# Kernel optimization log

Hardware: AMD Instinct MI355X
Metric: run time of the kernel (lower is better)

Reference implementation:

```python
import jax, jax.numpy as jnp
import numpy as np

EMBED_DIM = 256
NUM_HEADS = 8
NUM_LEVELS = 4
NUM_POINTS = 4
HEAD_DIM = EMBED_DIM // NUM_HEADS


def _bilinear_sample(img, x, y):
    """img: [N,C,H,W]; x,y: [N,P] absolute pixel coords (align_corners=False mapping
    already applied by caller). Zero padding outside, matching F.grid_sample."""
    N, C, H, W = img.shape
    x0 = jnp.floor(x)
    y0 = jnp.floor(y)
    wx1 = x - x0
    wy1 = y - y0
    img_flat = img.reshape(N, C, H * W)

    def gather(ix, iy):
        valid = ((ix >= 0) & (ix <= W - 1) & (iy >= 0) & (iy <= H - 1)).astype(img.dtype)
        idx = (jnp.clip(iy, 0, H - 1) * W + jnp.clip(ix, 0, W - 1)).astype(jnp.int32)
        v = jnp.take_along_axis(img_flat, idx[:, None, :], axis=2)  # [N,C,P]
        return v * valid[:, None, :]

    return (gather(x0, y0) * ((1.0 - wx1) * (1.0 - wy1))[:, None, :]
            + gather(x0 + 1.0, y0) * (wx1 * (1.0 - wy1))[:, None, :]
            + gather(x0, y0 + 1.0) * ((1.0 - wx1) * wy1)[:, None, :]
            + gather(x0 + 1.0, y0 + 1.0) * (wx1 * wy1)[:, None, :])


def _reference_points(H, W):
    yy, xx = jnp.meshgrid(jnp.arange(H, dtype=jnp.float32), jnp.arange(W, dtype=jnp.float32), indexing='ij')
    # stack order is (x, y), matching grid_sample's (x=width, y=height) convention
    return jnp.stack([(xx + 0.5) / W, (yy + 0.5) / H], axis=-1).reshape(H * W, 2)


def _frame_attention(q_feat, values, level_shapes, Wq, bq, Woff, boff, Wattn, battn, Wout, bout):
    Bt, C, H, W = q_feat.shape
    N = H * W
    q = q_feat.reshape(Bt, C, N).transpose(0, 2, 1) @ Wq + bq  # [Bt,N,C]
    off = (q @ Woff + boff).reshape(Bt, N, NUM_HEADS, NUM_LEVELS, NUM_POINTS, 2)
    aw = jax.nn.softmax((q @ Wattn + battn).reshape(Bt, N, NUM_HEADS, NUM_LEVELS * NUM_POINTS), axis=-1)
    aw = aw.reshape(Bt, N, NUM_HEADS, NUM_LEVELS, NUM_POINTS)
    ref = _reference_points(H, W)  # [N,2]
    sampled = []
    for l, (val, (Hl, Wl)) in enumerate(zip(values, level_shapes)):
        loc = ref[None, :, None, None, :] + off[:, :, :, l] / jnp.array([Wl, Hl], dtype=q.dtype)
        grid = jnp.clip(loc, 0.0, 1.0) * 2.0 - 1.0  # [Bt,N,M,K,2]
        grid = grid.transpose(0, 2, 1, 3, 4).reshape(Bt * NUM_HEADS, N * NUM_POINTS, 2)
        # align_corners=False: pixel = ((g+1)*size - 1)/2
        x = ((grid[..., 0] + 1.0) * Wl - 1.0) * 0.5
        y = ((grid[..., 1] + 1.0) * Hl - 1.0) * 0.5
        s = _bilinear_sample(val, x, y)  # [Bt*M, hd, N*K]
        s = s.reshape(Bt, NUM_HEADS, HEAD_DIM, N, NUM_POINTS).transpose(0, 3, 1, 4, 2)  # [Bt,N,M,K,hd]
        sampled.append(s)
    samp = jnp.stack(sampled, axis=3)  # [Bt,N,M,L,K,hd]
    out = (samp * aw[..., None]).sum(axis=(3, 4)).reshape(Bt, N, C)
    out = out @ Wout + bout
    return out.transpose(0, 2, 1).reshape(Bt, C, H, W)


def _forward(feats, Wq, bq, Wv, bv, Woff, boff, Wattn, battn, Wout, bout):
    B, C, H0, W0, T = feats[0].shape
    # original loops over frames t; frames are independent, so fold T into batch
    feats_bt = [jnp.moveaxis(f, -1, 1).reshape(f.shape[0] * T, C, f.shape[2], f.shape[3]) for f in feats]
    level_shapes = [(f.shape[2], f.shape[3]) for f in feats_bt]
    Bt = B * T
    # value projection per level (identical across query scales; compute once)
    values = []
    for f, (Hl, Wl) in zip(feats_bt, level_shapes):
        v = f.reshape(Bt, C, Hl * Wl).transpose(0, 2, 1) @ Wv + bv  # [Bt,HW,C]
        v = v.reshape(Bt, Hl * Wl, NUM_HEADS, HEAD_DIM).transpose(0, 2, 3, 1).reshape(Bt * NUM_HEADS, HEAD_DIM, Hl, Wl)
        values.append(v)
    outs = []
    for f, (Hl, Wl) in zip(feats_bt, level_shapes):
        o = _frame_attention(f, values, level_shapes, Wq, bq, Woff, boff, Wattn, battn, Wout, bout)
        outs.append(o.reshape(B, T, C, Hl, Wl).transpose(0, 2, 3, 4, 1))  # back to [B,C,H,W,T]
    return tuple(outs)


def setup_inputs() -> dict:
    key = jax.random.key(0)
    ks = jax.random.split(key, 10)
    B, T, C = 2, 2, EMBED_DIM
    shapes = [(64, 64), (32, 32), (16, 16), (8, 8)]
    inp = {}
    for i, (H, W) in enumerate(shapes):
        inp[f"feats{i}"] = jax.random.normal(ks[i], (B, C, H, W, T), dtype=jnp.float32)
    s = float(1.0 / np.sqrt(C))
    noff = NUM_HEADS * NUM_LEVELS * NUM_POINTS
    inp["Wq"] = jax.random.normal(ks[4], (C, C), jnp.float32) * s
    inp["bq"] = jnp.zeros((C,), jnp.float32)
    inp["Wv"] = jax.random.normal(ks[5], (C, C), jnp.float32) * s
    inp["bv"] = jnp.zeros((C,), jnp.float32)
    inp["Woff"] = jax.random.normal(ks[6], (C, noff * 2), jnp.float32) * 0.01
    inp["boff"] = jax.random.normal(ks[7], (noff * 2,), jnp.float32) * 2.0
    inp["Wattn"] = jax.random.normal(ks[8], (C, noff), jnp.float32) * 0.01
    inp["battn"] = jnp.zeros((noff,), jnp.float32)
    inp["Wout"] = jax.random.normal(ks[9], (C, C), jnp.float32) * s
    inp["bout"] = jnp.zeros((C,), jnp.float32)
    return inp


def reference(feats0, feats1, feats2, feats3, Wq, bq, Wv, bv, Woff, boff, Wattn, battn, Wout, bout):
    return _forward([feats0, feats1, feats2, feats3], Wq, bq, Wv, bv, Woff, boff, Wattn, battn, Wout, bout)
```

## Files before the change

kernel.cpp:

```cpp
#include <hip/hip_runtime.h>
#include <hip/hip_bf16.h>

#define NR 21760

typedef short short8 __attribute__((ext_vector_type(8)));
typedef float f32x4 __attribute__((ext_vector_type(4)));

__device__ __forceinline__ int level_of_row(int R) {
    if (R < 16384) return 0;
    if (R < 20480) return 1;
    if (R < 21504) return 2;
    return 3;
}

__global__ __launch_bounds__(256) void pack_all_kernel(const float* __restrict__ f0,
                                                       const float* __restrict__ f1,
                                                       const float* __restrict__ f2,
                                                       const float* __restrict__ f3,
                                                       __hip_bfloat16* __restrict__ XP) {
    int bx = blockIdx.x;
    const float* f; int nj, Wl, rowbase, rel;
    if (bx < 1024)      { f = f0; nj = 128; Wl = 64; rowbase = 0;     rel = bx; }
    else if (bx < 1280) { f = f1; nj = 32;  Wl = 32; rowbase = 16384; rel = bx - 1024; }
    else if (bx < 1344) { f = f2; nj = 8;   Wl = 16; rowbase = 20480; rel = bx - 1280; }
    else                { f = f3; nj = 2;   Wl = 8;  rowbase = 21504; rel = bx - 1344; }
    const int HW = Wl * Wl;
    const int HWT = HW * 2;
    const int j0 = (rel % nj) * 64;
    const int c0 = ((rel / nj) & 3) * 64;
    const int b  = rel / (nj * 4);
    __shared__ float tile[64][65];
    {
        const int tj = threadIdx.x & 63;
        const int tcb = threadIdx.x >> 6;
        const float* fb = f + (size_t)(b * 256 + c0) * HWT + j0;
#pragma unroll
        for (int i = 0; i < 16; ++i) {
            int cl = tcb + i * 4;
            tile[cl][tj] = fb[(size_t)cl * HWT + tj];
        }
    }
    __syncthreads();
    {
        const int tc = threadIdx.x & 63;
        const int tjb = threadIdx.x >> 6;
#pragma unroll
        for (int i = 0; i < 16; ++i) {
            int jl = tjb + i * 4;
            int j = j0 + jl;
            int p = j >> 1, t = j & 1;
            int row = rowbase + (b * 2 + t) * HW + p;
            XP[(size_t)row * 256 + c0 + tc] = __float2bfloat16(tile[tc][jl]);
        }
    }
}

__global__ __launch_bounds__(256) void wtrans_all_kernel(const float* __restrict__ Wq,
                                                         const float* __restrict__ Wv,
                                                         const float* __restrict__ Woff,
                                                         const float* __restrict__ Wattn,
                                                         const float* __restrict__ Wout,
                                                         const float* __restrict__ boff,
                                                         const float* __restrict__ battn,
                                                         __hip_bfloat16* __restrict__ WTvq,
                                                         __hip_bfloat16* __restrict__ WToa,
                                                         __hip_bfloat16* __restrict__ WTout,
                                                         float* __restrict__ bias_oa) {
    __shared__ float t[32][33];
    const int bx = blockIdx.x;
    const int tid = threadIdx.x;
    if (bx == 288) {
        bias_oa[tid] = boff[tid];
        if (tid < 128) bias_oa[256 + tid] = battn[tid];
        return;
    }
    const float* W; __hip_bfloat16* WT; int N; int rel;
    if (bx < 64)       { W = Wv;    WT = WTvq;             N = 256; rel = bx; }
    else if (bx < 128) { W = Wq;    WT = WTvq + 256 * 256; N = 256; rel = bx - 64; }
    else if (bx < 192) { W = Woff;  WT = WToa;             N = 256; rel = bx - 128; }
    else if (bx < 224) { W = Wattn; WT = WToa + 256 * 256; N = 128; rel = bx - 192; }
    else               { W = Wout;  WT = WTout;            N = 256; rel = bx - 224; }
    const int K = 256;
    const int ntiles = N >> 5;
    const int n0 = (rel % ntiles) * 32, k0 = (rel / ntiles) * 32;
    const int c = tid & 31, r = tid >> 5;
#pragma unroll
    for (int i = 0; i < 4; ++i)
        t[r + 8 * i][c] = W[(size_t)(k0 + r + 8 * i) * N + n0 + c];
    __syncthreads();
#pragma unroll
    for (int i = 0; i < 4; ++i)
        WT[(size_t)(n0 + r + 8 * i) * K + k0 + c] = __float2bfloat16(t[c][r + 8 * i]);
}

template <int OUTMODE>
__global__ __launch_bounds__(256) void gemm_mfma(const __hip_bfloat16* __restrict__ A,
                                                 const __hip_bfloat16* __restrict__ BT,
                                                 const float* __restrict__ bias,
                                                 const float* __restrict__ bias2,
                                                 void* __restrict__ Cout,
                                                 void* __restrict__ Cout2,
                                                 int M, int N, int K) {
    __shared__ __align__(16) __hip_bfloat16 As[64][72];
    __shared__ __align__(16) __hip_bfloat16 Bs[64][72];
    const int m0 = blockIdx.x * 64;
    const int n0 = blockIdx.y * 64;
    const int w = threadIdx.x >> 6;
    const int lane = threadIdx.x & 63;
    const int wm = (w >> 1) * 32;
    const int wn = (w & 1) * 32;
    const int fr = lane & 15;
    const int fq = lane >> 4;
    const int srow = threadIdx.x >> 3;
    const int schunk = threadIdx.x & 7;
    f32x4 acc[2][2] = {};

    for (int kt = 0; kt < K; kt += 64) {
        __syncthreads();
#pragma unroll
        for (int i = 0; i < 2; ++i) {
            int r = srow + 32 * i;
            float4 va = *(const float4*)(&A[(size_t)(m0 + r) * K + kt + schunk * 8]);
            *(float4*)(&As[r][schunk * 8]) = va;
            float4 vb = *(const float4*)(&BT[(size_t)(n0 + r) * K + kt + schunk * 8]);
            *(float4*)(&Bs[r][schunk * 8]) = vb;
        }
        __syncthreads();
#pragma unroll
        for (int ks = 0; ks < 2; ++ks) {
            short8 a[2], b[2];
#pragma unroll
            for (int fi = 0; fi < 2; ++fi)
                a[fi] = *(const short8*)(&As[wm + fi * 16 + fr][ks * 32 + fq * 8]);
#pragma unroll
            for (int fj = 0; fj < 2; ++fj)
                b[fj] = *(const short8*)(&Bs[wn + fj * 16 + fr][ks * 32 + fq * 8]);
#pragma unroll
            for (int fi = 0; fi < 2; ++fi)
#pragma unroll
                for (int fj = 0; fj < 2; ++fj)
                    acc[fi][fj] = __builtin_amdgcn_mfma_f32_16x16x32_bf16(
                        a[fi], b[fj], acc[fi][fj], 0, 0, 0);
        }
    }

    if (OUTMODE == 2) {
        const int lvl = level_of_row(m0);
        const int qbase[4]   = {0, 16384, 20480, 21504};
        const int wtab[4]    = {64, 32, 16, 8};
        const size_t obase[4] = {0, 4194304, 5242880, 5505024};
        const int Wl = wtab[lvl];
        const int HW = Wl * Wl;
        float* out = (float*)Cout;
#pragma unroll
        for (int fi = 0; fi < 2; ++fi)
#pragma unroll
            for (int fj = 0; fj < 2; ++fj) {
                int col = n0 + wn + fj * 16 + fr;
                float bb = bias[col];
#pragma unroll
                for (int r = 0; r < 4; ++r) {
                    int row = m0 + wm + fi * 16 + fq * 4 + r;
                    int r2 = row - qbase[lvl];
                    int bt = r2 / HW;
                    int p  = r2 - bt * HW;
                    int b  = bt >> 1, t = bt & 1;
                    int y  = p / Wl, x = p - y * Wl;
                    size_t addr = obase[lvl] +
                        ((((size_t)b * 256 + col) * Wl + y) * Wl + x) * 2 + t;
                    out[addr] = acc[fi][fj][r] + bb;
                }
            }
    } else if (OUTMODE == 1) {
        __hip_bfloat16* dst; const float* bs; int cb;
        if (n0 < 256) { dst = (__hip_bfloat16*)Cout;  bs = bias;  cb = n0; }
        else          { dst = (__hip_bfloat16*)Cout2; bs = bias2; cb = n0 - 256; }
#pragma unroll
        for (int fi = 0; fi < 2; ++fi)
#pragma unroll
            for (int fj = 0; fj < 2; ++fj) {
                int col = cb + wn + fj * 16 + fr;
                float bb = bs[col];
#pragma unroll
                for (int r = 0; r < 4; ++r) {
                    int row = m0 + wm + fi * 16 + fq * 4 + r;
                    dst[(size_t)row * 256 + col] = __float2bfloat16(acc[fi][fj][r] + bb);
                }
            }
    } else {
#pragma unroll
        for (int fi = 0; fi < 2; ++fi)
#pragma unroll
            for (int fj = 0; fj < 2; ++fj) {
                int col = n0 + wn + fj * 16 + fr;
                float bb = bias[col];
#pragma unroll
                for (int r = 0; r < 4; ++r) {
                    int row = m0 + wm + fi * 16 + fq * 4 + r;
                    ((float*)Cout)[(size_t)row * N + col] = acc[fi][fj][r] + bb;
                }
            }
    }
}

__device__ __forceinline__ void accum(f32x4& acc, uint2 u, float w) {
    acc[0] = fmaf(w, __uint_as_float(u.x << 16), acc[0]);
    acc[1] = fmaf(w, __uint_as_float(u.x & 0xffff0000u), acc[1]);
    acc[2] = fmaf(w, __uint_as_float(u.y << 16), acc[2]);
    acc[3] = fmaf(w, __uint_as_float(u.y & 0xffff0000u), acc[3]);
}

#define QB 4
__global__ __launch_bounds__(256, 2) void sample_kernel(const __hip_bfloat16* __restrict__ VAL,
                                                        const float* __restrict__ OA,
                                                        __hip_bfloat16* __restrict__ SAMP) {
    __shared__ int4   toff[QB * 16 * 8];
    __shared__ float4 twgt[QB * 16 * 8];
    const int R0 = blockIdx.x * QB;
    const int tid = threadIdx.x;
    const int qbase[4] = {0, 16384, 20480, 21504};
    const int wtab[4]  = {64, 32, 16, 8};

    if (tid < QB * 32) {
        const int qh = tid >> 2, part = tid & 3;
        const int q = qh >> 3, h = qh & 7;
        const int R = R0 + q;
        const int lq = level_of_row(R);
        const int Wq_ = wtab[lq];
        const int r2 = R - qbase[lq];
        const int bt = r2 / (Wq_ * Wq_);
        const int p  = r2 - bt * (Wq_ * Wq_);
        const float refx = ((p % Wq_) + 0.5f) / (float)Wq_;
        const float refy = ((p / Wq_) + 0.5f) / (float)Wq_;
        const float* oarow = OA + (size_t)R * 384;
        float4 offA = *(const float4*)(oarow + h * 32 + part * 8);
        float4 offB = *(const float4*)(oarow + h * 32 + part * 8 + 4);
        float4 awv  = *(const float4*)(oarow + 256 + h * 16 + part * 4);
        float m = fmaxf(fmaxf(awv.x, awv.y), fmaxf(awv.z, awv.w));
        m = fmaxf(m, __shfl_xor(m, 1));
        m = fmaxf(m, __shfl_xor(m, 2));
        float e0 = __expf(awv.x - m), e1 = __expf(awv.y - m);
        float e2 = __expf(awv.z - m), e3 = __expf(awv.w - m);
        float s = e0 + e1 + e2 + e3;
        s += __shfl_xor(s, 1);
        s += __shfl_xor(s, 2);
        const float inv = 1.0f / s;
        const int l = part;
        const int Wl = wtab[l];
        const float invWf = 1.0f / (float)Wl;
        const int base = (qbase[l] + bt * Wl * Wl) * 256;
        float oxy[8] = {offA.x, offA.y, offA.z, offA.w, offB.x, offB.y, offB.z, offB.w};
        float ee[4] = {e0, e1, e2, e3};
#pragma unroll
        for (int i = 0; i < 4; ++i) {
            float ox = oxy[2 * i], oy = oxy[2 * i + 1];
            float aw = ee[i] * inv;
            float lx = fminf(fmaxf(refx + ox * invWf, 0.f), 1.f);
            float ly = fminf(fmaxf(refy + oy * invWf, 0.f), 1.f);
            float px = lx * Wl - 0.5f;
            float py = ly * Wl - 0.5f;
            float x0f = floorf(px), y0f = floorf(py);
            int x0 = (int)x0f, y0 = (int)y0f;
            float wx = px - x0f, wy = py - y0f;
            float vx0 = (x0 >= 0) ? 1.f : 0.f;
            float vx1 = (x0 + 1 <= Wl - 1) ? 1.f : 0.f;
            float vy0 = (y0 >= 0) ? 1.f : 0.f;
            float vy1 = (y0 + 1 <= Wl - 1) ? 1.f : 0.f;
            int x0c = max(x0, 0), x1c = min(x0 + 1, Wl - 1);
            int y0c = max(y0, 0), y1c = min(y0 + 1, Wl - 1);
            int idx = (q * 16 + part * 4 + i) * 8 + h;
            toff[idx] = make_int4(base + (y0c * Wl + x0c) * 256,
                                  base + (y0c * Wl + x1c) * 256,
                                  base + (y1c * Wl + x0c) * 256,
                                  base + (y1c * Wl + x1c) * 256);
            float4 w4;
            w4.x = aw * (1.f - wx) * (1.f - wy) * vx0 * vy0;
            w4.y = aw * wx * (1.f - wy) * vx1 * vy0;
            w4.z = aw * (1.f - wx) * wy * vx0 * vy1;
            w4.w = aw * wx * wy * vx1 * vy1;
            twgt[idx] = w4;
        }
    }
    __syncthreads();

    const int wv = tid >> 6, lane = tid & 63;
    const int h = lane >> 3, d4 = lane & 7;
    const int R = R0 + wv;
    const __hip_bfloat16* vb = VAL + h * 32 + d4 * 4;
    const int4*   to = &toff[wv * 128];
    const float4* tw = &twgt[wv * 128];
    f32x4 acc = {0.f, 0.f, 0.f, 0.f};
#pragma unroll 2
    for (int t = 0; t < 16; ++t) {
        int4   o  = to[t * 8 + h];
        float4 w4 = tw[t * 8 + h];
        uint2 v00 = *(const uint2*)(vb + o.x);
        uint2 v10 = *(const uint2*)(vb + o.y);
        uint2 v01 = *(const uint2*)(vb + o.z);
        uint2 v11 = *(const uint2*)(vb + o.w);
        accum(acc, v00, w4.x);
        accum(acc, v10, w4.y);
        accum(acc, v01, w4.z);
        accum(acc, v11, w4.w);
    }
    union { ushort u[4]; ushort4 v4; } sa;
#pragma unroll
    for (int i = 0; i < 4; ++i) {
        __hip_bfloat16 ba = __float2bfloat16(acc[i]);
        sa.u[i] = *(ushort*)&ba;
    }
    *(ushort4*)(&SAMP[(size_t)R * 256 + h * 32 + d4 * 4]) = sa.v4;
}

extern "C" void kernel_launch(void* const* d_in, const int* in_sizes, int n_in,
                              void* d_out, int out_size, void* d_ws, size_t ws_size,
                              hipStream_t stream) {
    (void)in_sizes; (void)n_in; (void)out_size; (void)ws_size;
    const float* f0 = (const float*)d_in[0];
    const float* f1 = (const float*)d_in[1];
    const float* f2 = (const float*)d_in[2];
    const float* f3 = (const float*)d_in[3];
    const float* Wq    = (const float*)d_in[4];
    const float* bq    = (const float*)d_in[5];
    const float* Wv    = (const float*)d_in[6];
    const float* bv    = (const float*)d_in[7];
    const float* Woff  = (const float*)d_in[8];
    const float* boff  = (const float*)d_in[9];
    const float* Wattn = (const float*)d_in[10];
    const float* battn = (const float*)d_in[11];
    const float* Wout  = (const float*)d_in[12];
    const float* bout  = (const float*)d_in[13];
    float* out = (float*)d_out;

    char* w = (char*)d_ws;
    __hip_bfloat16* XPb   = (__hip_bfloat16*)w;   w += (size_t)NR * 256 * 2;
    __hip_bfloat16* Qb    = (__hip_bfloat16*)w;   w += (size_t)NR * 256 * 2;
    __hip_bfloat16* SAMPb = (__hip_bfloat16*)w;   w += (size_t)NR * 256 * 2;
    __hip_bfloat16* VAL   = (__hip_bfloat16*)w;   w += (size_t)NR * 256 * 2;
    float* OA   = (float*)w;                      w += (size_t)NR * 384 * 4;
    __hip_bfloat16* WTvq  = (__hip_bfloat16*)w;   w += 512 * 256 * 2;
    __hip_bfloat16* WToa  = (__hip_bfloat16*)w;   w += 384 * 256 * 2;
    __hip_bfloat16* WTout = (__hip_bfloat16*)w;   w += 256 * 256 * 2;
    float* bias_oa = (float*)w;                   w += 384 * 4;

    hipLaunchKernelGGL(pack_all_kernel, dim3(1360), dim3(256), 0, stream, f0, f1, f2, f3, XPb);

    hipLaunchKernelGGL(wtrans_all_kernel, dim3(289), dim3(256), 0, stream,
                       Wq, Wv, Woff, Wattn, Wout, boff, battn, WTvq, WToa, WTout, bias_oa);

    hipLaunchKernelGGL((gemm_mfma<1>), dim3(NR / 64, 8), dim3(256), 0, stream,
                       XPb, WTvq, bv, bq, (void*)VAL, (void*)Qb, NR, 512, 256);

    hipLaunchKernelGGL((gemm_mfma<0>), dim3(NR / 64, 6), dim3(256), 0, stream,
                       Qb, WToa, bias_oa, nullptr, (void*)OA, nullptr, NR, 384, 256);

    hipLaunchKernelGGL(sample_kernel, dim3(NR / QB), dim3(256), 0, stream, VAL, OA, SAMPb);

    hipLaunchKernelGGL((gemm_mfma<2>), dim3(NR / 64, 4), dim3(256), 0, stream,
                       SAMPb, WTout, bout, nullptr, (void*)out, nullptr, NR, 256, 256);
}
```

Measured before the change: 114.7 us.

## Fold query projection into offset/attention weights and widen sampling loads

Precomputes the product of the query projection with the offset and attention weights (plus folded biases), so the offset/attention GEMM reads the packed input directly. This removes the intermediate Q tensor and its write and read-back. The sampling kernel now stores each tap's offset and weight together and loads 8 bf16 values per lane, with shuffle reductions across corners. The folded weight is rounded to bf16 once, which changes the numerics slightly, and the bias fold runs as a serial 256-step dot product in a single block.

```diff
diff --git a/kernel.cpp b/kernel.cpp
--- a/kernel.cpp
+++ b/kernel.cpp
@@ -11,6 +11,11 @@
     if (R < 20480) return 1;
     if (R < 21504) return 2;
     return 3;
+}
+
+__device__ __forceinline__ unsigned pk2(float a, float b) {
+    __hip_bfloat16 x = __float2bfloat16(a), y = __float2bfloat16(b);
+    return (unsigned)*(unsigned short*)&x | ((unsigned)*(unsigned short*)&y << 16);
 }
 
 __global__ __launch_bounds__(256) void pack_all_kernel(const float* __restrict__ f0,
@@ -60,26 +65,47 @@
                                                          const float* __restrict__ Woff,
                                                          const float* __restrict__ Wattn,
                                                          const float* __restrict__ Wout,
+                                                         const float* __restrict__ bq,
                                                          const float* __restrict__ boff,
                                                          const float* __restrict__ battn,
-                                                         __hip_bfloat16* __restrict__ WTvq,
+                                                         __hip_bfloat16* __restrict__ WTv,
                                                          __hip_bfloat16* __restrict__ WToa,
+                                                         __hip_bfloat16* __restrict__ Wqb,
                                                          __hip_bfloat16* __restrict__ WTout,
                                                          float* __restrict__ bias_oa) {
-    __shared__ float t[32][33];
     const int bx = blockIdx.x;
     const int tid = threadIdx.x;
-    if (bx == 288) {
-        bias_oa[tid] = boff[tid];
-        if (tid < 128) bias_oa[256 + tid] = battn[tid];
+    if (bx == 256) {
+        {
+            int n = tid;
+            float s = 0.f;
+            for (int j = 0; j < 256; ++j) s += bq[j] * Woff[(size_t)j * 256 + n];
+            bias_oa[n] = s + boff[n];
+        }
+        if (tid < 128) {
+            int n = tid;
+            float s = 0.f;
+            for (int j = 0; j < 256; ++j) s += bq[j] * Wattn[(size_t)j * 128 + n];
+            bias_oa[256 + n] = s + battn[n];
+        }
         return;
     }
+    if (bx >= 160 && bx < 192) {
+        int e0 = (bx - 160) * 2048 + tid * 8;
+        float4 a = *(const float4*)(Wq + e0);
+        float4 b = *(const float4*)(Wq + e0 + 4);
+        uint4 o;
+        o.x = pk2(a.x, a.y); o.y = pk2(a.z, a.w);
+        o.z = pk2(b.x, b.y); o.w = pk2(b.z, b.w);
+        *(uint4*)(&Wqb[e0]) = o;
+        return;
+    }
+    __shared__ float t[32][33];
     const float* W; __hip_bfloat16* WT; int N; int rel;
-    if (bx < 64)       { W = Wv;    WT = WTvq;             N = 256; rel = bx; }
-    else if (bx < 128) { W = Wq;    WT = WTvq + 256 * 256; N = 256; rel = bx - 64; }
-    else if (bx < 192) { W = Woff;  WT = WToa;             N = 256; rel = bx - 128; }
-    else if (bx < 224) { W = Wattn; WT = WToa + 256 * 256; N = 128; rel = bx - 192; }
-    else               { W = Wout;  WT = WTout;            N = 256; rel = bx - 224; }
+    if (bx < 64)       { W = Wv;    WT = WTv;              N = 256; rel = bx; }
+    else if (bx < 128) { W = Woff;  WT = WToa;             N = 256; rel = bx - 64; }
+    else if (bx < 160) { W = Wattn; WT = WToa + 256 * 256; N = 128; rel = bx - 128; }
+    else               { W = Wout;  WT = WTout;            N = 256; rel = bx - 192; }
     const int K = 256;
     const int ntiles = N >> 5;
     const int n0 = (rel % ntiles) * 32, k0 = (rel / ntiles) * 32;
@@ -97,9 +123,7 @@
 __global__ __launch_bounds__(256) void gemm_mfma(const __hip_bfloat16* __restrict__ A,
                                                  const __hip_bfloat16* __restrict__ BT,
                                                  const float* __restrict__ bias,
-                                                 const float* __restrict__ bias2,
                                                  void* __restrict__ Cout,
-                                                 void* __restrict__ Cout2,
                                                  int M, int N, int K) {
     __shared__ __align__(16) __hip_bfloat16 As[64][72];
     __shared__ __align__(16) __hip_bfloat16 Bs[64][72];
@@ -171,67 +195,61 @@
                     out[addr] = acc[fi][fj][r] + bb;
                 }
             }
-    } else if (OUTMODE == 1) {
-        __hip_bfloat16* dst; const float* bs; int cb;
-        if (n0 < 256) { dst = (__hip_bfloat16*)Cout;  bs = bias;  cb = n0; }
-        else          { dst = (__hip_bfloat16*)Cout2; bs = bias2; cb = n0 - 256; }
+    } else {
 #pragma unroll
         for (int fi = 0; fi < 2; ++fi)
 #pragma unroll
             for (int fj = 0; fj < 2; ++fj) {
-                int col = cb + wn + fj * 16 + fr;
-                float bb = bs[col];
+                int col = n0 + wn + fj * 16 + fr;
+                float bb = bias ? bias[col] : 0.f;
 #pragma unroll
                 for (int r = 0; r < 4; ++r) {
                     int row = m0 + wm + fi * 16 + fq * 4 + r;
-                    dst[(size_t)row * 256 + col] = __float2bfloat16(acc[fi][fj][r] + bb);
+                    float v = acc[fi][fj][r] + bb;
+                    if (OUTMODE == 0)
+                        ((float*)Cout)[(size_t)row * N + col] = v;
+                    else
+                        ((__hip_bfloat16*)Cout)[(size_t)row * N + col] = __float2bfloat16(v);
                 }
             }
-    } else {
-#pragma unroll
-        for (int fi = 0; fi < 2; ++fi)
-#pragma unroll
-            for (int fj = 0; fj < 2; ++fj) {
-                int col = n0 + wn + fj * 16 + fr;
-                float bb = bias[col];
-#pragma unroll
-                for (int r = 0; r < 4; ++r) {
-                    int row = m0 + wm + fi * 16 + fq * 4 + r;
-                    ((float*)Cout)[(size_t)row * N + col] = acc[fi][fj][r] + bb;
-                }
-            }
-    }
-}
-
-__device__ __forceinline__ void accum(f32x4& acc, uint2 u, float w) {
-    acc[0] = fmaf(w, __uint_as_float(u.x << 16), acc[0]);
-    acc[1] = fmaf(w, __uint_as_float(u.x & 0xffff0000u), acc[1]);
-    acc[2] = fmaf(w, __uint_as_float(u.y << 16), acc[2]);
-    acc[3] = fmaf(w, __uint_as_float(u.y & 0xffff0000u), acc[3]);
+    }
+}
+
+__device__ __forceinline__ void acc8(f32x4& a, f32x4& b, uint4 v, float w) {
+    a[0] = fmaf(w, __uint_as_float(v.x << 16),          a[0]);
+    a[1] = fmaf(w, __uint_as_float(v.x & 0xffff0000u),  a[1]);
+    a[2] = fmaf(w, __uint_as_float(v.y << 16),          a[2]);
+    a[3] = fmaf(w, __uint_as_float(v.y & 0xffff0000u),  a[3]);
+    b[0] = fmaf(w, __uint_as_float(v.z << 16),          b[0]);
+    b[1] = fmaf(w, __uint_as_float(v.z & 0xffff0000u),  b[1]);
+    b[2] = fmaf(w, __uint_as_float(v.w << 16),          b[2]);
+    b[3] = fmaf(w, __uint_as_float(v.w & 0xffff0000u),  b[3]);
 }
 
 #define QB 4
 __global__ __launch_bounds__(256, 2) void sample_kernel(const __hip_bfloat16* __restrict__ VAL,
                                                         const float* __restrict__ OA,
                                                         __hip_bfloat16* __restrict__ SAMP) {
-    __shared__ int4   toff[QB * 16 * 8];
-    __shared__ float4 twgt[QB * 16 * 8];
+    __shared__ __align__(16) int2 tapd[QB * 512];
     const int R0 = blockIdx.x * QB;
     const int tid = threadIdx.x;
     const int qbase[4] = {0, 16384, 20480, 21504};
-    const int wtab[4]  = {64, 32, 16, 8};
+    const int wsh[4]   = {6, 5, 4, 3};
+    const int hwsh[4]  = {12, 10, 8, 6};
+    const float invwf[4] = {1.f/64.f, 1.f/32.f, 1.f/16.f, 1.f/8.f};
 
     if (tid < QB * 32) {
         const int qh = tid >> 2, part = tid & 3;
         const int q = qh >> 3, h = qh & 7;
         const int R = R0 + q;
         const int lq = level_of_row(R);
-        const int Wq_ = wtab[lq];
         const int r2 = R - qbase[lq];
-        const int bt = r2 / (Wq_ * Wq_);
-        const int p  = r2 - bt * (Wq_ * Wq_);
-        const float refx = ((p % Wq_) + 0.5f) / (float)Wq_;
-        const float refy = ((p / Wq_) + 0.5f) / (float)Wq_;
+        const int bt = r2 >> hwsh[lq];
+        const int p  = r2 & ((1 << hwsh[lq]) - 1);
+        const int pxi = p & ((1 << wsh[lq]) - 1);
+        const int pyi = p >> wsh[lq];
+        const float refx = (pxi + 0.5f) * invwf[lq];
+        const float refy = (pyi + 0.5f) * invwf[lq];
         const float* oarow = OA + (size_t)R * 384;
         float4 offA = *(const float4*)(oarow + h * 32 + part * 8);
         float4 offB = *(const float4*)(oarow + h * 32 + part * 8 + 4);
@@ -246,9 +264,9 @@
         s += __shfl_xor(s, 2);
         const float inv = 1.0f / s;
         const int l = part;
-        const int Wl = wtab[l];
-        const float invWf = 1.0f / (float)Wl;
-        const int base = (qbase[l] + bt * Wl * Wl) * 256;
+        const int Wl = 1 << wsh[l];
+        const float invWf = invwf[l];
+        const int base = (qbase[l] + (bt << hwsh[l])) << 8;
         float oxy[8] = {offA.x, offA.y, offA.z, offA.w, offB.x, offB.y, offB.z, offB.w};
         float ee[4] = {e0, e1, e2, e3};
 #pragma unroll
@@ -268,48 +286,55 @@
             float vy1 = (y0 + 1 <= Wl - 1) ? 1.f : 0.f;
             int x0c = max(x0, 0), x1c = min(x0 + 1, Wl - 1);
             int y0c = max(y0, 0), y1c = min(y0 + 1, Wl - 1);
-            int idx = (q * 16 + part * 4 + i) * 8 + h;
-            toff[idx] = make_int4(base + (y0c * Wl + x0c) * 256,
-                                  base + (y0c * Wl + x1c) * 256,
-                                  base + (y1c * Wl + x0c) * 256,
-                                  base + (y1c * Wl + x1c) * 256);
-            float4 w4;
-            w4.x = aw * (1.f - wx) * (1.f - wy) * vx0 * vy0;
-            w4.y = aw * wx * (1.f - wy) * vx1 * vy0;
-            w4.z = aw * (1.f - wx) * wy * vx0 * vy1;
-            w4.w = aw * wx * wy * vx1 * vy1;
-            twgt[idx] = w4;
+            int o00 = base + (((y0c << wsh[l]) + x0c) << 8);
+            int o10 = base + (((y0c << wsh[l]) + x1c) << 8);
+            int o01 = base + (((y1c << wsh[l]) + x0c) << 8);
+            int o11 = base + (((y1c << wsh[l]) + x1c) << 8);
+            float w00 = aw * (1.f - wx) * (1.f - wy) * vx0 * vy0;
+            float w10 = aw * wx * (1.f - wy) * vx1 * vy0;
+            float w01 = aw * (1.f - wx) * wy * vx0 * vy1;
+            float w11 = aw * wx * wy * vx1 * vy1;
+            int idx = ((q * 16 + part * 4 + i) * 8 + h) * 4;
+            *(int4*)(&tapd[idx])     = make_int4(o00, __float_as_int(w00), o10, __float_as_int(w10));
+            *(int4*)(&tapd[idx + 2]) = make_int4(o01, __float_as_int(w01), o11, __float_as_int(w11));
         }
     }
     __syncthreads();
 
-    const int wv = tid >> 6, lane = tid & 63;
-    const int h = lane >> 3, d4 = lane & 7;
-    const int R = R0 + wv;
-    const __hip_bfloat16* vb = VAL + h * 32 + d4 * 4;
-    const int4*   to = &toff[wv * 128];
-    const float4* tw = &twgt[wv * 128];
-    f32x4 acc = {0.f, 0.f, 0.f, 0.f};
+    const int wq = tid >> 6, lane = tid & 63;
+    const int u = lane >> 2, sub = lane & 3;
+    const int c = u & 3, h4 = u >> 2;
+    const int R = R0 + wq;
+    const __hip_bfloat16* v0base = VAL + h4 * 32 + sub * 8;
+    const __hip_bfloat16* v1base = VAL + (h4 + 4) * 32 + sub * 8;
+    const int2* tp = &tapd[wq * 512];
+    f32x4 aA0 = {0,0,0,0}, aA1 = {0,0,0,0};
+    f32x4 aB0 = {0,0,0,0}, aB1 = {0,0,0,0};
 #pragma unroll 2
     for (int t = 0; t < 16; ++t) {
-        int4   o  = to[t * 8 + h];
-        float4 w4 = tw[t * 8 + h];
-        uint2 v00 = *(const uint2*)(vb + o.x);
-        uint2 v10 = *(const uint2*)(vb + o.y);
-        uint2 v01 = *(const uint2*)(vb + o.z);
-        uint2 v11 = *(const uint2*)(vb + o.w);
-        accum(acc, v00, w4.x);
-        accum(acc, v10, w4.y);
-        accum(acc, v01, w4.z);
-        accum(acc, v11, w4.w);
-    }
-    union { ushort u[4]; ushort4 v4; } sa;
+        int2 d0 = tp[(t * 8 + h4) * 4 + c];
+        int2 d1 = tp[(t * 8 + h4 + 4) * 4 + c];
+        uint4 x0 = *(const uint4*)(v0base + d0.x);
+        uint4 x1 = *(const uint4*)(v1base + d1.x);
+        acc8(aA0, aA1, x0, __int_as_float(d0.y));
+        acc8(aB0, aB1, x1, __int_as_float(d1.y));
+    }
 #pragma unroll
     for (int i = 0; i < 4; ++i) {
-        __hip_bfloat16 ba = __float2bfloat16(acc[i]);
-        sa.u[i] = *(ushort*)&ba;
-    }
-    *(ushort4*)(&SAMP[(size_t)R * 256 + h * 32 + d4 * 4]) = sa.v4;
+        aA0[i] += __shfl_xor(aA0[i], 4); aA0[i] += __shfl_xor(aA0[i], 8);
+        aA1[i] += __shfl_xor(aA1[i], 4); aA1[i] += __shfl_xor(aA1[i], 8);
+        aB0[i] += __shfl_xor(aB0[i], 4); aB0[i] += __shfl_xor(aB0[i], 8);
+        aB1[i] += __shfl_xor(aB1[i], 4); aB1[i] += __shfl_xor(aB1[i], 8);
+    }
+    if (c == 0) {
+        uint4 o0, o1;
+        o0.x = pk2(aA0[0], aA0[1]); o0.y = pk2(aA0[2], aA0[3]);
+        o0.z = pk2(aA1[0], aA1[1]); o0.w = pk2(aA1[2], aA1[3]);
+        o1.x = pk2(aB0[0], aB0[1]); o1.y = pk2(aB0[2], aB0[3]);
+        o1.z = pk2(aB1[0], aB1[1]); o1.w = pk2(aB1[2], aB1[3]);
+        *(uint4*)(&SAMP[(size_t)R * 256 + h4 * 32 + sub * 8]) = o0;
+        *(uint4*)(&SAMP[(size_t)R * 256 + (h4 + 4) * 32 + sub * 8]) = o1;
+    }
 }
 
 extern "C" void kernel_launch(void* const* d_in, const int* in_sizes, int n_in,
@@ -334,28 +359,33 @@
 
     char* w = (char*)d_ws;
     __hip_bfloat16* XPb   = (__hip_bfloat16*)w;   w += (size_t)NR * 256 * 2;
-    __hip_bfloat16* Qb    = (__hip_bfloat16*)w;   w += (size_t)NR * 256 * 2;
     __hip_bfloat16* SAMPb = (__hip_bfloat16*)w;   w += (size_t)NR * 256 * 2;
     __hip_bfloat16* VAL   = (__hip_bfloat16*)w;   w += (size_t)NR * 256 * 2;
     float* OA   = (float*)w;                      w += (size_t)NR * 384 * 4;
-    __hip_bfloat16* WTvq  = (__hip_bfloat16*)w;   w += 512 * 256 * 2;
+    __hip_bfloat16* WTv   = (__hip_bfloat16*)w;   w += 256 * 256 * 2;
     __hip_bfloat16* WToa  = (__hip_bfloat16*)w;   w += 384 * 256 * 2;
+    __hip_bfloat16* Wqb   = (__hip_bfloat16*)w;   w += 256 * 256 * 2;
+    __hip_bfloat16* WpT   = (__hip_bfloat16*)w;   w += 384 * 256 * 2;
     __hip_bfloat16* WTout = (__hip_bfloat16*)w;   w += 256 * 256 * 2;
     float* bias_oa = (float*)w;                   w += 384 * 4;
 
     hipLaunchKernelGGL(pack_all_kernel, dim3(1360), dim3(256), 0, stream, f0, f1, f2, f3, XPb);
 
-    hipLaunchKernelGGL(wtrans_all_kernel, dim3(289), dim3(256), 0, stream,
-                       Wq, Wv, Woff, Wattn, Wout, boff, battn, WTvq, WToa, WTout, bias_oa);
-
-    hipLaunchKernelGGL((gemm_mfma<1>), dim3(NR / 64, 8), dim3(256), 0, stream,
-                       XPb, WTvq, bv, bq, (void*)VAL, (void*)Qb, NR, 512, 256);
+    hipLaunchKernelGGL(wtrans_all_kernel, dim3(257), dim3(256), 0, stream,
+                       Wq, Wv, Woff, Wattn, Wout, bq, boff, battn,
+                       WTv, WToa, Wqb, WTout, bias_oa);
+
+    hipLaunchKernelGGL((gemm_mfma<3>), dim3(6, 4), dim3(256), 0, stream,
+                       WToa, Wqb, nullptr, (void*)WpT, 384, 256, 256);
+
+    hipLaunchKernelGGL((gemm_mfma<3>), dim3(NR / 64, 4), dim3(256), 0, stream,
+                       XPb, WTv, bv, (void*)VAL, NR, 256, 256);
 
     hipLaunchKernelGGL((gemm_mfma<0>), dim3(NR / 64, 6), dim3(256), 0, stream,
-                       Qb, WToa, bias_oa, nullptr, (void*)OA, nullptr, NR, 384, 256);
+                       XPb, WpT, bias_oa, (void*)OA, NR, 384, 256);
 
     hipLaunchKernelGGL(sample_kernel, dim3(NR / QB), dim3(256), 0, stream, VAL, OA, SAMPb);
 
     hipLaunchKernelGGL((gemm_mfma<2>), dim3(NR / 64, 4), dim3(256), 0, stream,
-                       SAMPb, WTout, bout, nullptr, (void*)out, nullptr, NR, 256, 256);
-}
+                       SAMPb, WTout, bout, (void*)out, NR, 256, 256);
+}
```

Result: slower. 119.9 us (+4.5%).
